# Kernel optimization log

Measured on AMD Instinct MI355X. Metric: run time of the kernel, lower is better.

## Reference

```python
import jax, jax.numpy as jnp
import numpy as np

B, T, E, D, A = 32, 2048, 1024, 1024, 1024
SHARPENING = 1.0


def setup_inputs() -> dict:
    key = jax.random.key(0)
    ks = jax.random.split(key, 8)
    s = 0.02
    return {
        "enc_out": jax.random.normal(ks[0], (B, T, E), jnp.float32),
        "x_lens": jax.random.randint(ks[1], (B,), 1, T + 1, jnp.int32),
        "dec_out": jax.random.normal(ks[2], (B, 1, D), jnp.float32),
        "att_weights_step": jax.random.uniform(ks[3], (B, T), jnp.float32),
        "W_enc": jax.random.normal(ks[4], (E, A), jnp.float32) * s,
        "b_enc": jnp.zeros((A,), jnp.float32),
        "W_dec": jax.random.normal(ks[5], (D, A), jnp.float32) * s,
        "v": jax.random.normal(ks[6], (A,), jnp.float32) * s,
    }


def reference(enc_out, x_lens, dec_out, att_weights_step, W_enc, b_enc, W_dec, v):
    # content (Bahdanau additive) attention
    # energy[b,t] = v . tanh(W_enc enc[b,t] + b_enc + W_dec dec[b])
    enc_proj = jnp.einsum("bte,ea->bta", enc_out, W_enc) + b_enc  # [B,T,A]
    dec_proj = jnp.einsum("bod,da->boa", dec_out, W_dec)          # [B,1,A]
    energy = jnp.einsum("bta,a->bt", jnp.tanh(enc_proj + dec_proj), v)  # [B,T]
    # original multiplies energy by a 0/1 length mask (NOT -inf masking)
    mask = (jnp.arange(T)[None, :] < x_lens[:, None]).astype(energy.dtype)
    energy = energy * mask * SHARPENING
    att = jax.nn.softmax(energy, axis=-1)  # [B,T]
    context_vec = jnp.einsum("bte,bt->be", enc_out, att)[:, None, :]  # [B,1,E]
    return context_vec, att
```

## Files before the change

kernel.cpp:

```cpp
#include <hip/hip_runtime.h>
#include <hip/hip_bf16.h>
#include <stdint.h>


typedef __bf16 bf16;
typedef __bf16 bf16x8 __attribute__((ext_vector_type(8)));
typedef __bf16 bf16x4 __attribute__((ext_vector_type(4)));
typedef float floatx4 __attribute__((ext_vector_type(4)));

#define T_DIM 2048
#define B_DIM 32
#define K_DIM 1024
#define N_DIM 1024
#define M_DIM (B_DIM * T_DIM)
#define ENC_ELEMS ((size_t)M_DIM * K_DIM)

__device__ __forceinline__ void async_copy16(const bf16* g, bf16* l) {
    __builtin_amdgcn_global_load_lds(
        (const __attribute__((address_space(1))) void*)g,
        (__attribute__((address_space(3))) void*)l, 16, 0, 0);
}

__device__ __forceinline__ float fast_tanh(float x) {
    float ax = fabsf(x);
    float e  = __expf(ax + ax);
    float t  = 1.f - 2.f / (e + 1.f);
    return copysignf(t, x);
}

__global__ __launch_bounds__(256) void cvt_enc(const float* __restrict__ in,
                                               bf16* __restrict__ out) {
    size_t i = ((size_t)blockIdx.x * 256 + threadIdx.x) * 8;
    const size_t stride = (size_t)gridDim.x * 256 * 8;
    for (; i < ENC_ELEMS; i += stride) {
        float4 f0 = *(const float4*)(in + i);
        float4 f1 = *(const float4*)(in + i + 4);
        bf16x8 w;
        w[0] = (bf16)f0.x; w[1] = (bf16)f0.y; w[2] = (bf16)f0.z; w[3] = (bf16)f0.w;
        w[4] = (bf16)f1.x; w[5] = (bf16)f1.y; w[6] = (bf16)f1.z; w[7] = (bf16)f1.w;
        *(bf16x8*)(out + i) = w;
    }
}

__global__ __launch_bounds__(256) void transpose_wenc(
        const float* __restrict__ W, bf16* __restrict__ WT) {
    __shared__ bf16 tile[64][65];
    const int e0 = blockIdx.x * 64, a0 = blockIdx.y * 64;
    const int c = threadIdx.x & 63, r0 = threadIdx.x >> 6;
#pragma unroll
    for (int p = 0; p < 16; ++p) {
        int r = p * 4 + r0;
        tile[r][c] = (bf16)W[(size_t)(e0 + r) * 1024 + a0 + c];
    }
    __syncthreads();
#pragma unroll
    for (int p = 0; p < 16; ++p) {
        int r = p * 4 + r0;
        WT[(size_t)(a0 + r) * 1024 + e0 + c] = tile[c][r];
    }
}

__global__ __launch_bounds__(256) void decproj_kernel(
        const float* __restrict__ dec, const float* __restrict__ Wdec,
        const float* __restrict__ benc, float* __restrict__ dproj) {
    const int bg = blockIdx.x;
    const int a0 = blockIdx.y * 64;
    const int al = threadIdx.x & 63;
    const int dq = threadIdx.x >> 6;
    const int a  = a0 + al;
    __shared__ float sdec[8][1024];
    for (int i = threadIdx.x; i < 8192; i += 256)
        sdec[i >> 10][i & 1023] = dec[bg * 8192 + i];
    __syncthreads();
    float acc[8];
#pragma unroll
    for (int b = 0; b < 8; ++b) acc[b] = 0.f;
    for (int d = dq * 256; d < dq * 256 + 256; ++d) {
        const float w = Wdec[(size_t)d * 1024 + a];
#pragma unroll
        for (int b = 0; b < 8; ++b) acc[b] += sdec[b][d] * w;
    }
    __shared__ float red[4][8][64];
#pragma unroll
    for (int b = 0; b < 8; ++b) red[dq][b][al] = acc[b];
    __syncthreads();
    if (dq == 0) {
        const float be = benc[a];
#pragma unroll
        for (int b = 0; b < 8; ++b)
            dproj[(bg * 8 + b) * 1024 + a] =
                be + red[0][b][al] + red[1][b][al] + red[2][b][al] + red[3][b][al];
    }
}


#define HT 8192

#define BARRIER()  __builtin_amdgcn_s_barrier()
#define SCHEDB()   __builtin_amdgcn_sched_barrier(0)
#define VMCNT(n)   asm volatile("s_waitcnt vmcnt(" #n ")")

#define STAGE_A(kt, h, sl) {                                                   \
    const bf16* g_ = encb + (size_t)(m0 + (h)*128 + wave*8 + (lane>>3)) * 1024 \
                     + (kt)*64 + srccol;                                       \
    bf16* l_ = As + (((sl)*2 + (h)) * HT) + wave * 512;                        \
    async_copy16(g_, l_);                                                      \
    async_copy16(g_ + (size_t)64*1024, l_ + 4096);                             \
}
#define STAGE_B(kt, h) {                                                       \
    const bf16* g_ = WT + (size_t)(n0 + (h)*128 + wave*8 + (lane>>3)) * 1024   \
                     + (kt)*64 + srccol;                                       \
    bf16* l_ = Bs + ((((kt)&1)*2 + (h)) * HT) + wave * 512;                    \
    async_copy16(g_, l_);                                                      \
    async_copy16(g_ + (size_t)64*1024, l_ + 4096);                             \
}

#define PHASE(asl, tb, qm, qn, RA, STAGECODE, WAITCODE) {                      \
    const bf16* Ah_ = As + ((asl) * 2 + (qm)) * HT;                            \
    const bf16* Bh_ = Bs + ((tb) * 2 + (qn)) * HT;                             \
    if (RA) {                                                                  \
      _Pragma("unroll") for (int mf_ = 0; mf_ < 4; ++mf_) {                    \
        afr[mf_][0] = *(const bf16x8*)(Ah_ + (wm*64 + mf_*16 + lo)*64 + swz0); \
        afr[mf_][1] = *(const bf16x8*)(Ah_ + (wm*64 + mf_*16 + lo)*64 + swz1); \
      }                                                                        \
    }                                                                          \
    _Pragma("unroll") for (int nf_ = 0; nf_ < 2; ++nf_) {                      \
      bfr[nf_][0] = *(const bf16x8*)(Bh_ + (wn*32 + nf_*16 + lo)*64 + swz0);   \
      bfr[nf_][1] = *(const bf16x8*)(Bh_ + (wn*32 + nf_*16 + lo)*64 + swz1);   \
    }                                                                          \
    STAGECODE;                                                                 \
    SCHEDB();                                                                  \
    BARRIER();                                                                 \
    SCHEDB();                                                                  \
    __builtin_amdgcn_s_setprio(1);                                             \
    _Pragma("unroll") for (int kk_ = 0; kk_ < 2; ++kk_)                        \
      _Pragma("unroll") for (int mf_ = 0; mf_ < 4; ++mf_)                      \
        _Pragma("unroll") for (int nf_ = 0; nf_ < 2; ++nf_)                    \
          acc[qm][qn][mf_][nf_] = __builtin_amdgcn_mfma_f32_16x16x32_bf16(     \
              afr[mf_][kk_], bfr[nf_][kk_], acc[qm][qn][mf_][nf_], 0, 0, 0);   \
    __builtin_amdgcn_s_setprio(0);                                             \
    SCHEDB();                                                                  \
    WAITCODE;                                                                  \
    SCHEDB();                                                                  \
    BARRIER();                                                                 \
    SCHEDB();                                                                  \
}

__global__ __launch_bounds__(512, 2) void energy_gemm_8ph(
        const bf16* __restrict__ encb, const bf16* __restrict__ WT,
        const float* __restrict__ dproj, const float* __restrict__ v,
        float* __restrict__ part) {
    __shared__ __align__(16) bf16 As[6 * HT];
    __shared__ __align__(16) bf16 Bs[4 * HT];
    float* esum = (float*)As;

    const int tid  = threadIdx.x;
    const int lane = tid & 63;
    const int wave = tid >> 6;
    const int wm   = wave >> 2;
    const int wn   = wave & 3;
    const int lo   = lane & 15;
    const int hi   = lane >> 4;

    const int L = blockIdx.x;
    const int xcd  = L & 7;
    const int slot = L >> 3;
    const int m_tile  = xcd * 32 + (slot >> 2);
    const int n_chunk = slot & 3;
    const int m0 = m_tile * 256;
    const int n0 = n_chunk * 256;
    const int b  = m0 >> 11;

    const int srccol = (((lane & 7) ^ (lane >> 3)) << 3);
    const int swz0 = ((hi)     ^ (lo & 7)) << 3;
    const int swz1 = ((4 | hi) ^ (lo & 7)) << 3;

    floatx4 acc[2][2][4][2];
#pragma unroll
    for (int a_ = 0; a_ < 2; ++a_)
#pragma unroll
      for (int b_ = 0; b_ < 2; ++b_)
#pragma unroll
        for (int c_ = 0; c_ < 4; ++c_)
#pragma unroll
          for (int d_ = 0; d_ < 2; ++d_)
            acc[a_][b_][c_][d_] = (floatx4){0.f, 0.f, 0.f, 0.f};

    bf16x8 afr[4][2], bfr[2][2];

    float vv[2][2], dp[2][2];
#pragma unroll
    for (int qn = 0; qn < 2; ++qn)
#pragma unroll
      for (int nf = 0; nf < 2; ++nf) {
        int col = n0 + qn * 128 + wn * 32 + nf * 16 + lo;
        vv[qn][nf] = v[col];
        dp[qn][nf] = dproj[b * 1024 + col];
      }
    SCHEDB();
    VMCNT(0);
    SCHEDB();

    STAGE_B(0, 0); STAGE_B(0, 1);
    STAGE_A(0, 0, 0); STAGE_A(0, 1, 0);
    STAGE_A(1, 0, 1); STAGE_A(1, 1, 1);
    SCHEDB();
    VMCNT(4);
    SCHEDB();
    BARRIER();
    SCHEDB();

    int aslot = 0;
#pragma unroll 1
    for (int t = 0; t < 16; ++t) {
        const int tb   = t & 1;
        const int asl2 = (aslot >= 1) ? (aslot - 1) : 2;
        PHASE(aslot, tb, 0, 0, 1, { if (t < 15) STAGE_B(t + 1, 0); }, {});
        PHASE(aslot, tb, 0, 1, 0, { if (t < 15) STAGE_B(t + 1, 1); }, {});
        PHASE(aslot, tb, 1, 0, 1, { if (t < 14) STAGE_A(t + 2, 0, asl2); }, {});
        PHASE(aslot, tb, 1, 1, 0, { if (t < 14) STAGE_A(t + 2, 1, asl2); },
              { if (t < 14) { VMCNT(4); } else if (t == 14) { VMCNT(0); } });
        aslot = (aslot == 2) ? 0 : aslot + 1;
    }

    __syncthreads();
#pragma unroll
    for (int qm = 0; qm < 2; ++qm)
#pragma unroll
      for (int mf = 0; mf < 4; ++mf)
#pragma unroll
        for (int r = 0; r < 4; ++r) {
          float s = 0.f;
#pragma unroll
          for (int qn = 0; qn < 2; ++qn)
#pragma unroll
            for (int nf = 0; nf < 2; ++nf)
              s += vv[qn][nf] * fast_tanh(acc[qm][qn][mf][nf][r] + dp[qn][nf]);
          s += __shfl_xor(s, 1);
          s += __shfl_xor(s, 2);
          s += __shfl_xor(s, 4);
          s += __shfl_xor(s, 8);
          if (lo == 0)
            esum[wn * 256 + qm * 128 + wm * 64 + mf * 16 + hi * 4 + r] = s;
        }
    __syncthreads();
    if (tid < 256)
        part[(size_t)n_chunk * M_DIM + m0 + tid] =
            esum[tid] + esum[256 + tid] + esum[512 + tid] + esum[768 + tid];
}

__global__ __launch_bounds__(256) void energy_gemm_f32(
        const float* __restrict__ enc, const bf16* __restrict__ WT,
        const float* __restrict__ dproj, const float* __restrict__ v,
        float* __restrict__ part) {
    __shared__ __align__(16) bf16 As[128 * 32];
    __shared__ __align__(16) bf16 Bs[128 * 32];
    __shared__ float esum[128];

    const int tid  = threadIdx.x;
    const int lane = tid & 63;
    const int wave = tid >> 6;
    const int wy = wave >> 1, wx = wave & 1;
    const int L = blockIdx.x;
    const int xcd  = L & 7;
    const int slot = L >> 3;
    const int m_tile = xcd * 64 + (slot >> 3);
    const int n_chunk = slot & 7;
    const int m0 = m_tile * 128;
    const int n0 = n_chunk * 128;
    const int b  = m0 >> 11;

    if (tid < 128) esum[tid] = 0.f;

    floatx4 acc[4][4];
#pragma unroll
    for (int i = 0; i < 4; ++i)
#pragma unroll
        for (int j = 0; j < 4; ++j) acc[i][j] = (floatx4){0.f, 0.f, 0.f, 0.f};

    const int sr = tid >> 2;
    const int sc = (tid & 3) * 8;
    const float* gA = enc + (size_t)(m0 + sr) * 1024 + sc;
    const bf16*  gB = WT  + (size_t)(n0 + sr) * 1024 + sc;
    bf16* lA = As + sr * 32 + sc;
    bf16* lB = Bs + sr * 32 + sc;

    for (int k0 = 0; k0 < K_DIM; k0 += 32) {
        __syncthreads();
#pragma unroll
        for (int rep = 0; rep < 2; ++rep) {
            const float4* p = (const float4*)(gA + (size_t)rep * 64 * 1024 + k0);
            float4 f0 = p[0], f1 = p[1];
            bf16x8 w;
            w[0] = (bf16)f0.x; w[1] = (bf16)f0.y; w[2] = (bf16)f0.z; w[3] = (bf16)f0.w;
            w[4] = (bf16)f1.x; w[5] = (bf16)f1.y; w[6] = (bf16)f1.z; w[7] = (bf16)f1.w;
            *(bf16x8*)(lA + rep * 64 * 32) = w;
            *(bf16x8*)(lB + rep * 64 * 32) =
                *(const bf16x8*)(gB + (size_t)rep * 64 * 1024 + k0);
        }
        __syncthreads();

        bf16x8 af[4], bfrg[4];
#pragma unroll
        for (int i = 0; i < 4; ++i)
            af[i] = *(const bf16x8*)(As + (wy * 64 + i * 16 + (lane & 15)) * 32 + (lane >> 4) * 8);
#pragma unroll
        for (int i = 0; i < 4; ++i)
            bfrg[i] = *(const bf16x8*)(Bs + (wx * 64 + i * 16 + (lane & 15)) * 32 + (lane >> 4) * 8);
#pragma unroll
        for (int mi = 0; mi < 4; ++mi)
#pragma unroll
            for (int ni = 0; ni < 4; ++ni)
                acc[mi][ni] = __builtin_amdgcn_mfma_f32_16x16x32_bf16(
                    af[mi], bfrg[ni], acc[mi][ni], 0, 0, 0);
    }
    __syncthreads();

    float vv[4], dp[4];
#pragma unroll
    for (int ni = 0; ni < 4; ++ni) {
        int col = n0 + wx * 64 + ni * 16 + (lane & 15);
        vv[ni] = v[col];
        dp[ni] = dproj[b * 1024 + col];
    }
#pragma unroll
    for (int mi = 0; mi < 4; ++mi) {
#pragma unroll
        for (int r = 0; r < 4; ++r) {
            float s = 0.f;
#pragma unroll
            for (int ni = 0; ni < 4; ++ni)
                s += vv[ni] * fast_tanh(acc[mi][ni][r] + dp[ni]);
            s += __shfl_xor(s, 1);
            s += __shfl_xor(s, 2);
            s += __shfl_xor(s, 4);
            s += __shfl_xor(s, 8);
            if ((lane & 15) == 0) {
                int row = wy * 64 + mi * 16 + (lane >> 4) * 4 + r;
                atomicAdd(&esum[row], s);
            }
        }
    }
    __syncthreads();
    if (tid < 128) part[(size_t)n_chunk * M_DIM + m0 + tid] = esum[tid];
}

__global__ __launch_bounds__(256) void softmax_kernel(
        const float* __restrict__ part, const int* __restrict__ xlens,
        float* __restrict__ att, int nc) {
    const int b = blockIdx.x, tid = threadIdx.x;
    const int len = xlens[b];
    float e[8];
    float mx = -3.4e38f;
#pragma unroll
    for (int i = 0; i < 8; ++i) {
        const int t = tid + i * 256;
        float s = 0.f;
#pragma unroll 4
        for (int c = 0; c < nc; ++c) s += part[(size_t)c * M_DIM + b * 2048 + t];
        e[i] = (t < len) ? s : 0.f;
        mx = fmaxf(mx, e[i]);
    }
#pragma unroll
    for (int off = 1; off < 64; off <<= 1) mx = fmaxf(mx, __shfl_xor(mx, off));
    __shared__ float sr1[4], sr2[4];
    if ((tid & 63) == 0) sr1[tid >> 6] = mx;
    __syncthreads();
    mx = fmaxf(fmaxf(sr1[0], sr1[1]), fmaxf(sr1[2], sr1[3]));
    float sum = 0.f;
#pragma unroll
    for (int i = 0; i < 8; ++i) { e[i] = __expf(e[i] - mx); sum += e[i]; }
#pragma unroll
    for (int off = 1; off < 64; off <<= 1) sum += __shfl_xor(sum, off);
    if ((tid & 63) == 0) sr2[tid >> 6] = sum;
    __syncthreads();
    sum = sr2[0] + sr2[1] + sr2[2] + sr2[3];
    const float inv = 1.f / sum;
#pragma unroll
    for (int i = 0; i < 8; ++i)
        att[b * 2048 + tid + i * 256] = e[i] * inv;
}

__global__ __launch_bounds__(256) void context_part_kernel(
        const bf16* __restrict__ encb, const float* __restrict__ att,
        float* __restrict__ ctxpart) {
    const int b = blockIdx.x, chunk = blockIdx.y, tid = threadIdx.x;
    const int t0 = chunk * 128;
    __shared__ float satt[128];
    if (tid < 128) satt[tid] = att[b * 2048 + t0 + tid];
    __syncthreads();
    const bf16* base = encb + ((size_t)b * 2048 + t0) * 1024 + tid * 4;
    float a0 = 0.f, a1 = 0.f, a2 = 0.f, a3 = 0.f;
#pragma unroll 4
    for (int t = 0; t < 128; ++t) {
        bf16x4 ev = *(const bf16x4*)(base + (size_t)t * 1024);
        float w = satt[t];
        a0 += w * (float)ev[0]; a1 += w * (float)ev[1];
        a2 += w * (float)ev[2]; a3 += w * (float)ev[3];
    }
    float* o = ctxpart + ((size_t)b * 16 + chunk) * 1024 + tid * 4;
    o[0] = a0; o[1] = a1; o[2] = a2; o[3] = a3;
}

__global__ __launch_bounds__(256) void context_reduce_kernel(
        const float* __restrict__ ctxpart, float* __restrict__ out_ctx) {
    const int i = blockIdx.x * 256 + threadIdx.x;
    const int b = i >> 10, e = i & 1023;
    const float* p = ctxpart + (size_t)b * 16 * 1024 + e;
    float s = 0.f;
#pragma unroll
    for (int c = 0; c < 16; ++c) s += p[c * 1024];
    out_ctx[i] = s;
}

__global__ __launch_bounds__(256) void context_kernel_f32(
        const float* __restrict__ enc, const float* __restrict__ att,
        float* __restrict__ ctx) {
    const int b = blockIdx.x, t0 = blockIdx.y * 128, tid = threadIdx.x;
    __shared__ float satt[128];
    if (tid < 128) satt[tid] = att[b * 2048 + t0 + tid];
    __syncthreads();
    const float* base = enc + ((size_t)b * 2048 + t0) * 1024 + tid * 4;
    float a0 = 0.f, a1 = 0.f, a2 = 0.f, a3 = 0.f;
    for (int t = 0; t < 128; ++t) {
        float4 ev = *(const float4*)(base + (size_t)t * 1024);
        float w = satt[t];
        a0 += w * ev.x; a1 += w * ev.y; a2 += w * ev.z; a3 += w * ev.w;
    }
    float* o = ctx + b * 1024 + tid * 4;
    atomicAdd(o + 0, a0); atomicAdd(o + 1, a1);
    atomicAdd(o + 2, a2); atomicAdd(o + 3, a3);
}

extern "C" void kernel_launch(void* const* d_in, const int* in_sizes, int n_in,
                              void* d_out, int out_size, void* d_ws, size_t ws_size,
                              hipStream_t stream) {
    const float* enc   = (const float*)d_in[0];
    const int*   xlens = (const int*)d_in[1];
    const float* dec   = (const float*)d_in[2];
    const float* Wenc  = (const float*)d_in[4];
    const float* benc  = (const float*)d_in[5];
    const float* Wdec  = (const float*)d_in[6];
    const float* v     = (const float*)d_in[7];

    float* out_ctx = (float*)d_out;
    float* out_att = out_ctx + B_DIM * K_DIM;

    char* ws = (char*)d_ws;
    float* dproj   = (float*)ws;
    bf16*  WT      = (bf16*)(ws + (128u << 10));
    float* part    = (float*)(ws + (128u << 10) + (2u << 20));
    bf16*  encb    = (bf16*)(ws + (128u << 10) + (4u << 20));
    float* ctxpart = (float*)(ws + (128u << 10) + (4u << 20) + (ENC_ELEMS * 2));
    const size_t need = (128u << 10) + (4u << 20) + ENC_ELEMS * 2 + (2u << 21);

    transpose_wenc<<<dim3(16, 16), 256, 0, stream>>>(Wenc, WT);
    decproj_kernel<<<dim3(4, 16), 256, 0, stream>>>(dec, Wdec, benc, dproj);

    if (ws_size >= need) {
        cvt_enc<<<2048, 256, 0, stream>>>(enc, encb);
        energy_gemm_8ph<<<1024, 512, 0, stream>>>(encb, WT, dproj, v, part);
        softmax_kernel<<<B_DIM, 256, 0, stream>>>(part, xlens, out_att, 4);
        context_part_kernel<<<dim3(B_DIM, 16), 256, 0, stream>>>(encb, out_att, ctxpart);
        context_reduce_kernel<<<B_DIM * K_DIM / 256, 256, 0, stream>>>(ctxpart, out_ctx);
    } else {
        hipMemsetAsync(out_ctx, 0, B_DIM * K_DIM * sizeof(float), stream);
        energy_gemm_f32<<<4096, 256, 0, stream>>>(enc, WT, dproj, v, part);
        softmax_kernel<<<B_DIM, 256, 0, stream>>>(part, xlens, out_att, 8);
        context_kernel_f32<<<dim3(B_DIM, 16), 256, 0, stream>>>(enc, out_att, out_ctx);
    }
}
```

Before: 613.5 us.

## Collapse four barrier-separated GEMM phases into two halves per K-tile

```diff
diff --git a/kernel.cpp b/kernel.cpp
--- a/kernel.cpp
+++ b/kernel.cpp
@@ -115,37 +115,6 @@
     async_copy16(g_ + (size_t)64*1024, l_ + 4096);                             \
 }
 
-#define PHASE(asl, tb, qm, qn, RA, STAGECODE, WAITCODE) {                      \
-    const bf16* Ah_ = As + ((asl) * 2 + (qm)) * HT;                            \
-    const bf16* Bh_ = Bs + ((tb) * 2 + (qn)) * HT;                             \
-    if (RA) {                                                                  \
-      _Pragma("unroll") for (int mf_ = 0; mf_ < 4; ++mf_) {                    \
-        afr[mf_][0] = *(const bf16x8*)(Ah_ + (wm*64 + mf_*16 + lo)*64 + swz0); \
-        afr[mf_][1] = *(const bf16x8*)(Ah_ + (wm*64 + mf_*16 + lo)*64 + swz1); \
-      }                                                                        \
-    }                                                                          \
-    _Pragma("unroll") for (int nf_ = 0; nf_ < 2; ++nf_) {                      \
-      bfr[nf_][0] = *(const bf16x8*)(Bh_ + (wn*32 + nf_*16 + lo)*64 + swz0);   \
-      bfr[nf_][1] = *(const bf16x8*)(Bh_ + (wn*32 + nf_*16 + lo)*64 + swz1);   \
-    }                                                                          \
-    STAGECODE;                                                                 \
-    SCHEDB();                                                                  \
-    BARRIER();                                                                 \
-    SCHEDB();                                                                  \
-    __builtin_amdgcn_s_setprio(1);                                             \
-    _Pragma("unroll") for (int kk_ = 0; kk_ < 2; ++kk_)                        \
-      _Pragma("unroll") for (int mf_ = 0; mf_ < 4; ++mf_)                      \
-        _Pragma("unroll") for (int nf_ = 0; nf_ < 2; ++nf_)                    \
-          acc[qm][qn][mf_][nf_] = __builtin_amdgcn_mfma_f32_16x16x32_bf16(     \
-              afr[mf_][kk_], bfr[nf_][kk_], acc[qm][qn][mf_][nf_], 0, 0, 0);   \
-    __builtin_amdgcn_s_setprio(0);                                             \
-    SCHEDB();                                                                  \
-    WAITCODE;                                                                  \
-    SCHEDB();                                                                  \
-    BARRIER();                                                                 \
-    SCHEDB();                                                                  \
-}
-
 __global__ __launch_bounds__(512, 2) void energy_gemm_8ph(
         const bf16* __restrict__ encb, const bf16* __restrict__ WT,
         const float* __restrict__ dproj, const float* __restrict__ v,
@@ -186,8 +155,6 @@
           for (int d_ = 0; d_ < 2; ++d_)
             acc[a_][b_][c_][d_] = (floatx4){0.f, 0.f, 0.f, 0.f};
 
-    bf16x8 afr[4][2], bfr[2][2];
-
     float vv[2][2], dp[2][2];
 #pragma unroll
     for (int qn = 0; qn < 2; ++qn)
@@ -208,18 +175,71 @@
     VMCNT(4);
     SCHEDB();
     BARRIER();
-    SCHEDB();
 
     int aslot = 0;
 #pragma unroll 1
     for (int t = 0; t < 16; ++t) {
         const int tb   = t & 1;
         const int asl2 = (aslot >= 1) ? (aslot - 1) : 2;
-        PHASE(aslot, tb, 0, 0, 1, { if (t < 15) STAGE_B(t + 1, 0); }, {});
-        PHASE(aslot, tb, 0, 1, 0, { if (t < 15) STAGE_B(t + 1, 1); }, {});
-        PHASE(aslot, tb, 1, 0, 1, { if (t < 14) STAGE_A(t + 2, 0, asl2); }, {});
-        PHASE(aslot, tb, 1, 1, 0, { if (t < 14) STAGE_A(t + 2, 1, asl2); },
-              { if (t < 14) { VMCNT(4); } else if (t == 14) { VMCNT(0); } });
+        const bf16* Bh0 = Bs + (tb * 2 + 0) * HT;
+        const bf16* Bh1 = Bs + (tb * 2 + 1) * HT;
+        const bf16* Ah0 = As + (aslot * 2 + 0) * HT;
+        const bf16* Ah1 = As + (aslot * 2 + 1) * HT;
+
+        bf16x8 bfr[2][2][2], af0[4][2], af1[4][2];
+#pragma unroll
+        for (int qn = 0; qn < 2; ++qn) {
+            const bf16* Bh_ = qn ? Bh1 : Bh0;
+#pragma unroll
+            for (int nf = 0; nf < 2; ++nf) {
+                bfr[qn][nf][0] = *(const bf16x8*)(Bh_ + (wn*32 + nf*16 + lo)*64 + swz0);
+                bfr[qn][nf][1] = *(const bf16x8*)(Bh_ + (wn*32 + nf*16 + lo)*64 + swz1);
+            }
+        }
+#pragma unroll
+        for (int mf = 0; mf < 4; ++mf) {
+            af0[mf][0] = *(const bf16x8*)(Ah0 + (wm*64 + mf*16 + lo)*64 + swz0);
+            af0[mf][1] = *(const bf16x8*)(Ah0 + (wm*64 + mf*16 + lo)*64 + swz1);
+        }
+        if (t < 15) { STAGE_B(t + 1, 0); STAGE_B(t + 1, 1); }
+
+        __builtin_amdgcn_s_setprio(1);
+#pragma unroll
+        for (int kk = 0; kk < 2; ++kk)
+#pragma unroll
+          for (int mf = 0; mf < 4; ++mf)
+#pragma unroll
+            for (int qn = 0; qn < 2; ++qn)
+#pragma unroll
+              for (int nf = 0; nf < 2; ++nf)
+                acc[0][qn][mf][nf] = __builtin_amdgcn_mfma_f32_16x16x32_bf16(
+                    af0[mf][kk], bfr[qn][nf][kk], acc[0][qn][mf][nf], 0, 0, 0);
+        __builtin_amdgcn_s_setprio(0);
+
+#pragma unroll
+        for (int mf = 0; mf < 4; ++mf) {
+            af1[mf][0] = *(const bf16x8*)(Ah1 + (wm*64 + mf*16 + lo)*64 + swz0);
+            af1[mf][1] = *(const bf16x8*)(Ah1 + (wm*64 + mf*16 + lo)*64 + swz1);
+        }
+        if (t < 14) { STAGE_A(t + 2, 0, asl2); STAGE_A(t + 2, 1, asl2); }
+
+        __builtin_amdgcn_s_setprio(1);
+#pragma unroll
+        for (int kk = 0; kk < 2; ++kk)
+#pragma unroll
+          for (int mf = 0; mf < 4; ++mf)
+#pragma unroll
+            for (int qn = 0; qn < 2; ++qn)
+#pragma unroll
+              for (int nf = 0; nf < 2; ++nf)
+                acc[1][qn][mf][nf] = __builtin_amdgcn_mfma_f32_16x16x32_bf16(
+                    af1[mf][kk], bfr[qn][nf][kk], acc[1][qn][mf][nf], 0, 0, 0);
+        __builtin_amdgcn_s_setprio(0);
+
+        SCHEDB();
+        if (t < 14) { VMCNT(4); } else if (t == 14) { VMCNT(0); }
+        SCHEDB();
+        BARRIER();
         aslot = (aslot == 2) ? 0 : aslot + 1;
     }
 
```

New measurement: 582.2 us. 1.05x faster.
